# Performance work log

Hardware: AMD Instinct MI355X
Metric: run time of the kernel (lower is better)

The kernel has to match this reference:

```python
import jax, jax.numpy as jnp
import numpy as np

NQ = 4  # n_qubits
C64 = jnp.complex64
INV_SQRT2 = np.float32(1.0 / np.sqrt(2.0))
H_GATE = jnp.array([[1.0, 1.0], [1.0, -1.0]], dtype=C64) * INV_SQRT2


def _apply_1q(state, U, q):
    # state: (B, 2,2,2,2) complex; U: (2,2) shared or (B,2,2) per-batch
    s = jnp.moveaxis(state, q + 1, -1)
    if U.ndim == 2:
        s = jnp.einsum('b...i,ji->b...j', s, U)
    else:
        s = jnp.einsum('b...i,bji->b...j', s, U)
    return jnp.moveaxis(s, -1, q + 1)


def _apply_cnot(state, c, t):
    s = jnp.moveaxis(state, (c + 1, t + 1), (-2, -1))
    s = jnp.stack([s[..., 0, :], s[..., 1, ::-1]], axis=-2)  # flip target when control=1
    return jnp.moveaxis(s, (-2, -1), (c + 1, t + 1))


def _ry(theta):
    co = jnp.cos(theta * 0.5).astype(C64)
    si = jnp.sin(theta * 0.5).astype(C64)
    return jnp.stack([jnp.stack([co, -si], -1), jnp.stack([si, co], -1)], -2)


def _rz(theta):
    e = jnp.exp(-0.5j * theta).astype(C64)
    z = jnp.zeros_like(e)
    return jnp.stack([jnp.stack([e, z], -1), jnp.stack([z, jnp.conj(e)], -1)], -2)


def _rx(theta):
    co = jnp.cos(theta * 0.5).astype(C64)
    si = (-1j * jnp.sin(theta * 0.5)).astype(C64)
    return jnp.stack([jnp.stack([co, si], -1), jnp.stack([si, co], -1)], -2)


def _vqc(y, w):
    # y: (B, NQ) float angles-to-encode; w: (n_qlayers, 3, NQ)
    B = y.shape[0]
    state = jnp.zeros((B, 2 ** NQ), C64).at[:, 0].set(1.0).reshape((B,) + (2,) * NQ)
    ry_ang = jnp.arctan(y)
    rz_ang = jnp.arctan(y * y)
    # encoding: H, RY(arctan y), RZ(arctan y^2) on each wire
    for q in range(NQ):
        state = _apply_1q(state, H_GATE, q)
        state = _apply_1q(state, _ry(ry_ang[:, q]), q)
        state = _apply_1q(state, _rz(rz_ang[:, q]), q)
    # ansatz layers: CNOT ring (n_esteps=1), then RX/RY/RZ with weights
    for l in range(w.shape[0]):
        for q in range(NQ):
            state = _apply_cnot(state, q, (q + 1) % NQ)
        for q in range(NQ):
            state = _apply_1q(state, _rx(w[l, 0, q]), q)
            state = _apply_1q(state, _ry(w[l, 1, q]), q)
            state = _apply_1q(state, _rz(w[l, 2, q]), q)
    probs = state.real ** 2 + state.imag ** 2  # (B,2,2,2,2)
    outs = []
    for q in range(NQ):
        p = jnp.moveaxis(probs, q + 1, 1).reshape(B, 2, -1).sum(-1)
        outs.append(p[:, 0] - p[:, 1])  # <Z_q>
    return jnp.stack(outs, -1).astype(y.dtype)


def _qlstm(x, W_in, b_in, W_out, b_out, w_f, w_i, w_u, w_o):
    B = x.shape[0]
    Hdim = W_out.shape[1]
    h0 = jnp.zeros((B, Hdim), x.dtype)
    c0 = jnp.zeros((B, Hdim), x.dtype)

    def step(carry, x_t):
        h, c = carry
        y = jnp.concatenate([h, x_t], axis=1) @ W_in + b_in  # (B, NQ)
        f = jax.nn.sigmoid(_vqc(y, w_f) @ W_out + b_out)
        i = jax.nn.sigmoid(_vqc(y, w_i) @ W_out + b_out)
        g = jnp.tanh(_vqc(y, w_u) @ W_out + b_out)
        o = jax.nn.sigmoid(_vqc(y, w_o) @ W_out + b_out)
        c = f * c + i * g
        h = o * jnp.tanh(c)
        return (h, c), h

    (hT, cT), outs = jax.lax.scan(step, (h0, c0), jnp.swapaxes(x, 0, 1))
    return jnp.swapaxes(outs, 0, 1), hT, cT


def setup_inputs() -> dict:
    key = jax.random.key(0)
    ks = jax.random.split(key, 9)
    B, S, D, Hdim = 512, 256, 64, 128
    x = jax.random.normal(ks[0], (B, S, D), jnp.float32)
    W_in = jax.random.normal(ks[1], (Hdim + D, NQ), jnp.float32) * 0.1
    b_in = jax.random.normal(ks[2], (NQ,), jnp.float32) * 0.1
    W_out = jax.random.normal(ks[3], (NQ, Hdim), jnp.float32) * 0.1
    b_out = jax.random.normal(ks[4], (Hdim,), jnp.float32) * 0.1
    two_pi = np.float32(2.0 * np.pi)
    w_f = jax.random.uniform(ks[5], (1, 3, NQ), jnp.float32, 0.0, two_pi)
    w_i = jax.random.uniform(ks[6], (1, 3, NQ), jnp.float32, 0.0, two_pi)
    w_u = jax.random.uniform(ks[7], (1, 3, NQ), jnp.float32, 0.0, two_pi)
    w_o = jax.random.uniform(ks[8], (1, 3, NQ), jnp.float32, 0.0, two_pi)
    return {'x': x, 'W_in': W_in, 'b_in': b_in, 'W_out': W_out, 'b_out': b_out,
            'w_f': w_f, 'w_i': w_i, 'w_u': w_u, 'w_o': w_o}


def reference(x, W_in, b_in, W_out, b_out, w_f, w_i, w_u, w_o):
    return _qlstm(x, W_in, b_in, W_out, b_out, w_f, w_i, w_u, w_o)
```

## Files before the change

### kernel.cpp

```cpp
#include <hip/hip_runtime.h>
#include <math.h>

#define B_TOT 512
#define S_LEN 256
#define D_IN  64
#define HDIM  128

__device__ __forceinline__ float rcp_f(float x) { return __builtin_amdgcn_rcpf(x); }
__device__ __forceinline__ float rsq_f(float x) { return __builtin_amdgcn_rsqf(x); }
__device__ __forceinline__ float sig_f(float x) { return rcp_f(1.0f + __expf(-x)); }
__device__ __forceinline__ float tanh_f(float x) { return 1.0f - 2.0f * rcp_f(1.0f + __expf(2.0f * x)); }

template<int CTRL>
__device__ __forceinline__ float dpp_add(float v) {
    int t = __builtin_amdgcn_update_dpp(0, __float_as_int(v), CTRL, 0xF, 0xF, true);
    return v + __int_as_float(t);
}

__device__ __forceinline__ float allsum64(float v) {
    v = dpp_add<0xB1>(v);
    v = dpp_add<0x4E>(v);
    v = dpp_add<0x141>(v);
    v = dpp_add<0x140>(v);
    int r0 = __builtin_amdgcn_readlane(__float_as_int(v), 0);
    int r1 = __builtin_amdgcn_readlane(__float_as_int(v), 16);
    int r2 = __builtin_amdgcn_readlane(__float_as_int(v), 32);
    int r3 = __builtin_amdgcn_readlane(__float_as_int(v), 48);
    return (__int_as_float(r0) + __int_as_float(r1))
         + (__int_as_float(r2) + __int_as_float(r3));
}

__global__ void __launch_bounds__(64, 1) qlstm_kernel(
    const float* __restrict__ x,
    const float* __restrict__ Win,
    const float* __restrict__ bin,
    const float* __restrict__ Wout,
    const float* __restrict__ bout,
    const float* __restrict__ wf,
    const float* __restrict__ wi,
    const float* __restrict__ wu,
    const float* __restrict__ wo,
    float* __restrict__ out)
{
    const int b = blockIdx.x;
    const int l = threadIdx.x;

    const float4* W4 = reinterpret_cast<const float4*>(Win);
    const float4 wh0 = W4[l];
    const float4 wh1 = W4[64 + l];
    const float4 wx  = W4[128 + l];
    const float4 bn  = *reinterpret_cast<const float4*>(bin);

    float Wo0[4], Wo1[4];
#pragma unroll
    for (int q = 0; q < 4; ++q) {
        Wo0[q] = Wout[q * HDIM + l];
        Wo1[q] = Wout[q * HDIM + 64 + l];
    }
    const float bo0 = bout[l];
    const float bo1 = bout[64 + l];

    float U[4][4][3];
    {
        const float* wg[4] = {wf, wi, wu, wo};
#pragma unroll
        for (int g = 0; g < 4; ++g) {
#pragma unroll
            for (int q = 0; q < 4; ++q) {
                float a  = wg[g][q];
                float be = wg[g][4 + q];
                float sa = sinf(a),  ca = cosf(a);
                float sb = sinf(be), cb = cosf(be);
                U[g][q][0] = -sb;
                U[g][q][1] = cb * sa;
                U[g][q][2] = cb * ca;
            }
        }
    }

    float h0 = 0.f, h1 = 0.f, c0 = 0.f, c1 = 0.f;

    const float* xb = x + (size_t)b * (S_LEN * D_IN) + l;
    float* ob = out + (size_t)b * (S_LEN * HDIM) + l;

    float xa  = xb[0];
    float xnb = xb[D_IN];
    float xc0 = xa * wx.x, xc1 = xa * wx.y, xc2 = xa * wx.z, xc3 = xa * wx.w;

    for (int t = 0; t < S_LEN; ++t) {
        const int tl = (t + 2 < S_LEN) ? (t + 2) : (S_LEN - 1);
        float xnew = xb[(size_t)tl * D_IN];

        float p0 = fmaf(h0, wh0.x, fmaf(h1, wh1.x, xc0));
        float p1 = fmaf(h0, wh0.y, fmaf(h1, wh1.y, xc1));
        float p2 = fmaf(h0, wh0.z, fmaf(h1, wh1.z, xc2));
        float p3 = fmaf(h0, wh0.w, fmaf(h1, wh1.w, xc3));
        float y0 = allsum64(p0) + bn.x;
        float y1 = allsum64(p1) + bn.y;
        float y2 = allsum64(p2) + bn.z;
        float y3 = allsum64(p3) + bn.w;

        xc0 = xnb * wx.x; xc1 = xnb * wx.y; xc2 = xnb * wx.z; xc3 = xnb * wx.w;

        float nx[4], ny[4], nz[4];
        float ys[4] = {y0, y1, y2, y3};
#pragma unroll
        for (int q = 0; q < 4; ++q) {
            float y   = ys[q];
            float y2s = y * y;
            float r1  = rsq_f(fmaf(y, y, 1.0f));
            float r2  = rsq_f(fmaf(y2s, y2s, 1.0f));
            float xx  = r1 * r2;
            nx[q] = xx;
            ny[q] = y2s * xx;
            nz[q] = -y * r1;
        }

        float nz01 = nz[0] * nz[1];
        float nz23 = nz[2] * nz[3];
        float TX[4], TY[4], TZ[4];
        TX[0] = nx[0] * nx[1];
        TX[1] = nx[1] * nx[2];
        TX[2] = nx[2] * nx[3];
        TX[3] = TX[0] * nx[3];
        TZ[0] = nz[1] * nz23;
        TZ[1] = nz01;
        TZ[2] = nz01 * nz[2];
        TZ[3] = nz01 * nz23;
        TY[0] = (nx[0] * ny[1]) * nz23;
        TY[1] = (nz[0] * ny[1]) * nx[2];
        TY[2] = (nz01 * ny[2]) * nx[3];
        TY[3] = -(ny[0] * ny[1]) * (nz[2] * ny[3]);

        float pre0[4], pre1[4];
#pragma unroll
        for (int g = 0; g < 4; ++g) {
            float s0 = bo0, s1 = bo1;
#pragma unroll
            for (int q = 0; q < 4; ++q) {
                float z = fmaf(U[g][q][0], TX[q],
                          fmaf(U[g][q][1], TY[q],
                               U[g][q][2] * TZ[q]));
                s0 = fmaf(z, Wo0[q], s0);
                s1 = fmaf(z, Wo1[q], s1);
            }
            pre0[g] = s0; pre1[g] = s1;
        }

        float f0 = sig_f(pre0[0]),  f1 = sig_f(pre1[0]);
        float i0 = sig_f(pre0[1]),  i1 = sig_f(pre1[1]);
        float g0 = tanh_f(pre0[2]), g1 = tanh_f(pre1[2]);
        float o0 = sig_f(pre0[3]),  o1 = sig_f(pre1[3]);
        c0 = fmaf(f0, c0, i0 * g0);
        c1 = fmaf(f1, c1, i1 * g1);
        h0 = o0 * tanh_f(c0);
        h1 = o1 * tanh_f(c1);

        ob[(size_t)t * HDIM]      = h0;
        ob[(size_t)t * HDIM + 64] = h1;

        xa = xnb; xnb = xnew;
    }

    float* hT = out + (size_t)B_TOT * S_LEN * HDIM;
    float* cT = hT + (size_t)B_TOT * HDIM;
    hT[(size_t)b * HDIM + l]      = h0;
    hT[(size_t)b * HDIM + 64 + l] = h1;
    cT[(size_t)b * HDIM + l]      = c0;
    cT[(size_t)b * HDIM + 64 + l] = c1;
}

extern "C" void kernel_launch(void* const* d_in, const int* in_sizes, int n_in,
                              void* d_out, int out_size, void* d_ws, size_t ws_size,
                              hipStream_t stream) {
    qlstm_kernel<<<dim3(B_TOT), dim3(64), 0, stream>>>(
        (const float*)d_in[0],
        (const float*)d_in[1],
        (const float*)d_in[2],
        (const float*)d_in[3],
        (const float*)d_in[4],
        (const float*)d_in[5],
        (const float*)d_in[6],
        (const float*)d_in[7],
        (const float*)d_in[8],
        (float*)d_out);
}
```

Measured before the change: 237.0 us.

## Unroll recurrence by four with batched x prefetch and deferred output stores

The time loop is processed in groups of four steps. The next group's x values are prefetched one group ahead, and each group's h outputs are buffered and written during the following group, which moves global loads and stores off the serial dependency chain. The input bias is pre-scaled by 1/64 and folded into each lane's partial sum before the cross-lane reduction, removing one add from the critical path. This costs more registers and changes the floating-point summation order slightly.

```diff
diff --git a/kernel.cpp b/kernel.cpp
--- a/kernel.cpp
+++ b/kernel.cpp
@@ -49,7 +49,9 @@
     const float4 wh0 = W4[l];
     const float4 wh1 = W4[64 + l];
     const float4 wx  = W4[128 + l];
-    const float4 bn  = *reinterpret_cast<const float4*>(bin);
+    const float4 bn4 = *reinterpret_cast<const float4*>(bin);
+    const float bn0 = bn4.x * 0.015625f, bn1 = bn4.y * 0.015625f,
+                bn2 = bn4.z * 0.015625f, bn3 = bn4.w * 0.015625f;
 
     float Wo0[4], Wo1[4];
 #pragma unroll
@@ -83,27 +85,22 @@
     const float* xb = x + (size_t)b * (S_LEN * D_IN) + l;
     float* ob = out + (size_t)b * (S_LEN * HDIM) + l;
 
-    float xa  = xb[0];
-    float xnb = xb[D_IN];
-    float xc0 = xa * wx.x, xc1 = xa * wx.y, xc2 = xa * wx.z, xc3 = xa * wx.w;
-
-    for (int t = 0; t < S_LEN; ++t) {
-        const int tl = (t + 2 < S_LEN) ? (t + 2) : (S_LEN - 1);
-        float xnew = xb[(size_t)tl * D_IN];
-
+    auto step = [&](float xval) {
+        float xc0 = fmaf(xval, wx.x, bn0);
+        float xc1 = fmaf(xval, wx.y, bn1);
+        float xc2 = fmaf(xval, wx.z, bn2);
+        float xc3 = fmaf(xval, wx.w, bn3);
         float p0 = fmaf(h0, wh0.x, fmaf(h1, wh1.x, xc0));
         float p1 = fmaf(h0, wh0.y, fmaf(h1, wh1.y, xc1));
         float p2 = fmaf(h0, wh0.z, fmaf(h1, wh1.z, xc2));
         float p3 = fmaf(h0, wh0.w, fmaf(h1, wh1.w, xc3));
-        float y0 = allsum64(p0) + bn.x;
-        float y1 = allsum64(p1) + bn.y;
-        float y2 = allsum64(p2) + bn.z;
-        float y3 = allsum64(p3) + bn.w;
-
-        xc0 = xnb * wx.x; xc1 = xnb * wx.y; xc2 = xnb * wx.z; xc3 = xnb * wx.w;
+        float ys[4];
+        ys[0] = allsum64(p0);
+        ys[1] = allsum64(p1);
+        ys[2] = allsum64(p2);
+        ys[3] = allsum64(p3);
 
         float nx[4], ny[4], nz[4];
-        float ys[4] = {y0, y1, y2, y3};
 #pragma unroll
         for (int q = 0; q < 4; ++q) {
             float y   = ys[q];
@@ -155,11 +152,57 @@
         c1 = fmaf(f1, c1, i1 * g1);
         h0 = o0 * tanh_f(c0);
         h1 = o1 * tanh_f(c1);
-
-        ob[(size_t)t * HDIM]      = h0;
-        ob[(size_t)t * HDIM + 64] = h1;
-
-        xa = xnb; xnb = xnew;
+    };
+
+    float xg[4], xn[4];
+#pragma unroll
+    for (int j = 0; j < 4; ++j) {
+        xg[j] = xb[(size_t)j * D_IN];
+        xn[j] = xb[(size_t)(4 + j) * D_IN];
+    }
+
+    float ph0[4], ph1[4];
+
+#pragma unroll
+    for (int j = 0; j < 4; ++j) {
+        step(xg[j]);
+        ph0[j] = h0; ph1[j] = h1;
+    }
+
+    for (int g = 1; g < S_LEN / 4; ++g) {
+        const int tprev = (g - 1) * 4;
+        float* op = ob + (size_t)tprev * HDIM;
+#pragma unroll
+        for (int j = 0; j < 4; ++j) {
+            op[(size_t)j * HDIM]      = ph0[j];
+            op[(size_t)j * HDIM + 64] = ph1[j];
+        }
+#pragma unroll
+        for (int j = 0; j < 4; ++j) xg[j] = xn[j];
+#pragma unroll
+        for (int j = 0; j < 4; ++j) {
+            int tn = (g + 1) * 4 + j;
+            if (tn > S_LEN - 1) tn = S_LEN - 1;
+            xn[j] = xb[(size_t)tn * D_IN];
+        }
+        float nh0[4], nh1[4];
+#pragma unroll
+        for (int j = 0; j < 4; ++j) {
+            step(xg[j]);
+            nh0[j] = h0; nh1[j] = h1;
+        }
+#pragma unroll
+        for (int j = 0; j < 4; ++j) { ph0[j] = nh0[j]; ph1[j] = nh1[j]; }
+    }
+
+    {
+        const int tprev = S_LEN - 4;
+        float* op = ob + (size_t)tprev * HDIM;
+#pragma unroll
+        for (int j = 0; j < 4; ++j) {
+            op[(size_t)j * HDIM]      = ph0[j];
+            op[(size_t)j * HDIM + 64] = ph1[j];
+        }
     }
 
     float* hT = out + (size_t)B_TOT * S_LEN * HDIM;
```

Result: faster. 229.7 us (-3.1%).
